# Performance work log

Measured on AMD Instinct MI355X. Metric: run time of the kernel, lower is better.

The kernel has to match this reference:

```python
import jax, jax.numpy as jnp
import numpy as np
from jax import lax

STRIDES = (8, 16, 32)
FEAT_SIZES = ((80, 80), (40, 40), (20, 20))  # 640x640 input
NUM_CLASSES = 80
NMS_THR = 0.65
SCORE_THR = 0.01
NMS_PRE = 1000
MAX_PER_IMG = 100


def make_points():
    # MlvlPointGenerator.grid_priors with offset=0, with_stride=True.
    pts = []
    for (h, w), s in zip(FEAT_SIZES, STRIDES):
        y, x = jnp.meshgrid(jnp.arange(h, dtype=jnp.float32),
                            jnp.arange(w, dtype=jnp.float32), indexing='ij')
        pts.append(jnp.stack([x.ravel() * s, y.ravel() * s,
                              jnp.full(h * w, float(s)),
                              jnp.full(h * w, float(s))], axis=-1))
    return jnp.concatenate(pts, axis=0)  # [P, 4] = (px, py, sx, sy)


def decode_boxes(points, reg):
    # YOLOXBBoxDecoder: xy = reg[:2]*stride + point; wh = exp(reg[2:])*stride
    xys = reg[..., :2] * points[..., 2:] + points[..., :2]
    whs = jnp.exp(reg[..., 2:]) * points[..., 2:]
    half = whs * 0.5
    return jnp.concatenate([xys - half, xys + half], axis=-1)  # [..., 4] xyxy


def pairwise_iou(b):
    # b: [N, 4] xyxy
    area = (b[:, 2] - b[:, 0]) * (b[:, 3] - b[:, 1])
    lt = jnp.maximum(b[:, None, :2], b[None, :, :2])
    rb = jnp.minimum(b[:, None, 2:], b[None, :, 2:])
    wh = jnp.clip(rb - lt, 0.0)
    inter = wh[..., 0] * wh[..., 1]
    return inter / (area[:, None] + area[None, :] - inter + 1e-9)


def nms_image(cls_s, boxes, obj):
    # cls_s: [P, C] sigmoid scores, boxes: [P, 4], obj: [P] sigmoid objectness
    max_scores = jnp.max(cls_s, axis=-1)
    labels = jnp.argmax(cls_s, axis=-1)
    scores = max_scores * obj
    masked = jnp.where(scores >= SCORE_THR, scores, -1.0)
    top_scores, top_idx = lax.top_k(masked, NMS_PRE)  # sorted descending
    valid = top_scores >= SCORE_THR
    b = boxes[top_idx]            # [K, 4]
    lab = labels[top_idx]         # [K]
    # batched_nms: offset boxes per class so cross-class boxes never overlap
    off = lab.astype(b.dtype)[:, None] * (jnp.max(jnp.abs(b)) + 1.0)
    iou = pairwise_iou(b + off)   # [K, K]
    idx = jnp.arange(NMS_PRE)

    def body(i, keep):
        sup = (iou[i] > NMS_THR) & keep[i] & (idx > i)
        return keep & ~sup

    keep = lax.fori_loop(0, NMS_PRE, body, valid)
    # compact kept detections (score-sorted order preserved), pad to MAX_PER_IMG
    order = jnp.argsort(~keep, stable=True)[:MAX_PER_IMG]
    k = keep[order]
    out_b = jnp.where(k[:, None], b[order], 0.0)
    out_s = jnp.where(k, top_scores[order], 0.0)
    out_l = jnp.where(k, lab[order], -1)
    return out_b, out_s, out_l


def setup_inputs() -> dict:
    key = jax.random.key(0)
    ks = jax.random.split(key, 9)
    shapes = {
        'cls0': (32, NUM_CLASSES, 80, 80), 'cls1': (32, NUM_CLASSES, 40, 40),
        'cls2': (32, NUM_CLASSES, 20, 20),
        'reg0': (32, 4, 80, 80), 'reg1': (32, 4, 40, 40), 'reg2': (32, 4, 20, 20),
        'obj0': (32, 1, 80, 80), 'obj1': (32, 1, 40, 40), 'obj2': (32, 1, 20, 20),
    }
    return {n: jax.random.normal(k, s, dtype=jnp.float32)
            for (n, s), k in zip(shapes.items(), ks)}


def reference(cls0, cls1, cls2, reg0, reg1, reg2, obj0, obj1, obj2):
    def flat(xs, c):
        return jnp.concatenate(
            [jnp.transpose(x, (0, 2, 3, 1)).reshape(x.shape[0], -1, c) for x in xs],
            axis=1)
    cls = flat([cls0, cls1, cls2], NUM_CLASSES)   # [N, P, C]
    reg = flat([reg0, reg1, reg2], 4)             # [N, P, 4]
    obj = flat([obj0, obj1, obj2], 1)[..., 0]     # [N, P]
    points = make_points()                        # [P, 4]
    boxes = decode_boxes(points[None], reg)       # [N, P, 4]
    cls = jax.nn.sigmoid(cls)
    obj = jax.nn.sigmoid(obj)
    return jax.vmap(nms_image)(cls, boxes, obj)   # ([N,M,4],[N,M],[N,M] labels)
```

## Files before the change

kernel.cpp:

```cpp
#include <hip/hip_runtime.h>
#include <stdint.h>

#define N_IMG 32
#define P_TOT 8400
#define NCLS 80
#define NMS_PRE 1000
#define MAXOUT 100
#define SCORE_THRF 0.01f
#define NMS_THRF 0.65f
#define CAND_N 2048
#define NB 512
#define BINBASE 8192
#define TIE_EPS 0.05f


__device__ __forceinline__ float sigmoidf_(float x) { return 1.0f / (1.0f + expf(-x)); }

__global__ __launch_bounds__(256) void k_score(
    const float* __restrict__ cls0, const float* __restrict__ cls1, const float* __restrict__ cls2,
    const float* __restrict__ obj0, const float* __restrict__ obj1, const float* __restrict__ obj2,
    uint64_t* __restrict__ keys)
{
    __shared__ float    pml[4][64];
    __shared__ uint64_t part[4][64];
    int lane = threadIdx.x & 63, wid = threadIdx.x >> 6;
    int a = blockIdx.x * 64 + lane;
    int n = a / P_TOT;
    int p = a - n * P_TOT;

    const float* cl; const float* ob; int HW, q;
    if (p < 6400)      { cl = cls0; ob = obj0; HW = 6400; q = p; }
    else if (p < 8000) { cl = cls1; ob = obj1; HW = 1600; q = p - 6400; }
    else               { cl = cls2; ob = obj2; HW = 400;  q = p - 8000; }

    const float* cbase = cl + (size_t)n * NCLS * HW + q;
    int c0 = wid * 20;

    float lg[20];
    #pragma unroll
    for (int i = 0; i < 20; ++i)
        lg[i] = cbase[(size_t)(c0 + i) * HW];
    __builtin_amdgcn_sched_group_barrier(0x20, 20, 0);

    float a0 = fmaxf(lg[0], lg[1]),  a1 = fmaxf(lg[2], lg[3]);
    float a2 = fmaxf(lg[4], lg[5]),  a3 = fmaxf(lg[6], lg[7]);
    float a4 = fmaxf(lg[8], lg[9]),  a5 = fmaxf(lg[10], lg[11]);
    float a6 = fmaxf(lg[12], lg[13]), a7 = fmaxf(lg[14], lg[15]);
    float a8 = fmaxf(lg[16], lg[17]), a9 = fmaxf(lg[18], lg[19]);
    float b0 = fmaxf(a0, a1), b1 = fmaxf(a2, a3), b2 = fmaxf(a4, a5);
    float b3 = fmaxf(a6, a7), b4 = fmaxf(a8, a9);
    float lmax = fmaxf(fmaxf(fmaxf(b0, b1), fmaxf(b2, b3)), b4);
    pml[wid][lane] = lmax;
    __syncthreads();

    float gmaxl = fmaxf(fmaxf(pml[0][lane], pml[1][lane]),
                        fmaxf(pml[2][lane], pml[3][lane]));
    float thr = gmaxl - TIE_EPS;
    uint64_t m = 0;
    #pragma unroll
    for (int i = 0; i < 20; ++i) {
        if (lg[i] >= thr) {
            float s = sigmoidf_(lg[i]);
            uint64_t pk = ((uint64_t)__float_as_uint(s) << 8) | (uint32_t)(79 - (c0 + i));
            m = m > pk ? m : pk;
        }
    }
    part[wid][lane] = m;
    __syncthreads();

    if (wid == 0) {
        uint64_t m0 = part[0][lane], m1 = part[1][lane];
        uint64_t m2 = part[2][lane], m3 = part[3][lane];
        uint64_t ma = m0 > m1 ? m0 : m1, mb = m2 > m3 ? m2 : m3;
        uint64_t mm = ma > mb ? ma : mb;
        float best = __uint_as_float((uint32_t)(mm >> 8));
        int bc = 79 - (int)(mm & 0xFFu);

        float so = sigmoidf_(ob[(size_t)n * HW + q]);
        float sc = __fmul_rn(best, so);
        float masked = (sc >= SCORE_THRF) ? sc : -1.0f;
        uint32_t u = __float_as_uint(masked);
        uint32_t ord = (u & 0x80000000u) ? ~u : (u | 0x80000000u);
        uint32_t dk = ~ord;
        keys[a] = ((uint64_t)dk << 32) | (uint32_t)((p << 8) | bc);
    }
}

__global__ __launch_bounds__(1024) void k_selnms(
    const uint64_t* __restrict__ keys,
    const float* __restrict__ reg0, const float* __restrict__ reg1, const float* __restrict__ reg2,
    float* __restrict__ out)
{
    __shared__ __align__(16) char big[55712];
    __shared__ int   s_misc[2];
    __shared__ float fsh[17];
    __shared__ int   kidx[MAXOUT];

    uint16_t* bin16   = (uint16_t*)big;
    uint32_t* hist    = (uint32_t*)(big + 16800);
    uint32_t* base    = (uint32_t*)(big + 18848);
    uint32_t* fill    = (uint32_t*)(big + 20896);
    uint64_t* grouped = (uint64_t*)(big + 22944);
    uint64_t* cand    = (uint64_t*)(big + 39328);
    float4* s_obx = (float4*)big;
    float*  s_oar = (float*) (big + 16000);
    float4* s_raw = (float4*)(big + 20000);
    float2* s_sl  = (float2*)(big + 36000);

    int n = blockIdx.x, tid = threadIdx.x;
    const uint64_t* kbase = keys + (size_t)n * P_TOT;

    if (tid < NB) { hist[tid] = 0; fill[tid] = 0; }
    for (int t = tid; t < CAND_N; t += 1024) cand[t] = ~0ull;
    __syncthreads();

    #pragma unroll
    for (int it = 0; it < 9; ++it) {
        int t = tid + it * 1024;
        if (t < P_TOT) {
            uint64_t k = kbase[t];
            uint32_t dk = (uint32_t)(k >> 32);
            uint16_t v = 0;
            if (!(dk & 0x80000000u)) {
                uint32_t bin = (dk >> 17) - BINBASE;
                atomicAdd(&hist[bin], 1u);
                v = (uint16_t)(bin + 1);
            }
            bin16[t] = v;
        }
    }
    __syncthreads();

    if (tid < 64) {
        uint32_t c[8]; uint32_t s = 0;
        #pragma unroll
        for (int i = 0; i < 8; ++i) { c[i] = hist[tid * 8 + i]; s += c[i]; }
        uint32_t inc = s;
        #pragma unroll
        for (int o = 1; o < 64; o <<= 1) {
            uint32_t v = __shfl_up(inc, o);
            if (tid >= o) inc += v;
        }
        uint32_t excl = inc - s;
        uint32_t b = excl;
        #pragma unroll
        for (int i = 0; i < 8; ++i) { base[tid * 8 + i] = b; b += c[i]; }
        uint32_t total = __shfl(inc, 63);
        uint32_t target = total < (uint32_t)NMS_PRE ? total : (uint32_t)NMS_PRE;
        uint32_t cum = excl; int found = 0x7fffffff;
        #pragma unroll
        for (int i = 0; i < 8; ++i) {
            cum += c[i];
            if (found == 0x7fffffff && cum >= target && target > 0) found = tid * 8 + i;
        }
        #pragma unroll
        for (int o = 32; o > 0; o >>= 1) { int f = __shfl_xor(found, o); found = f < found ? f : found; }
        if (tid == 0) { s_misc[0] = (total > 0) ? found : -1; s_misc[1] = (int)target; }
    }
    __syncthreads();
    int Bcut = s_misc[0];

    #pragma unroll
    for (int it = 0; it < 9; ++it) {
        int t = tid + it * 1024;
        if (t < P_TOT) {
            uint16_t v = bin16[t];
            if (v != 0) {
                int bin = (int)v - 1;
                if (bin <= Bcut) {
                    uint32_t pos = base[bin] + atomicAdd(&fill[bin], 1u);
                    if (pos < CAND_N) grouped[pos] = kbase[t];
                }
            }
        }
    }
    __syncthreads();

    int ccnt = 0;
    if (Bcut >= 0) {
        uint32_t cc = base[Bcut] + hist[Bcut];
        ccnt = cc < (uint32_t)CAND_N ? (int)cc : CAND_N;
    }
    for (int s = tid; s < ccnt; s += 1024) {
        uint64_t k = grouped[s];
        uint32_t dk = (uint32_t)(k >> 32);
        int bin = (int)((dk >> 17) - BINBASE);
        uint32_t b0 = base[bin];
        uint32_t e0 = b0 + hist[bin]; if (e0 > (uint32_t)CAND_N) e0 = CAND_N;
        uint32_t r = b0;
        for (uint32_t t = b0; t < e0; ++t) r += (grouped[t] < k) ? 1u : 0u;
        if (r < (uint32_t)CAND_N) cand[r] = k;
    }
    int V = s_misc[1];
    __syncthreads();

    float4 bx = make_float4(0.f, 0.f, 0.f, 0.f);
    float scm = -1.0f, labf = 0.f, m = 0.f;
    if (tid < NMS_PRE) {
        uint64_t key = cand[tid];
        uint32_t dk = (uint32_t)(key >> 32);
        if (!(dk & 0x80000000u)) {
            uint32_t low = (uint32_t)key;
            int lab = (int)(low & 0xFFu);
            int p   = (int)(low >> 8);
            uint32_t ord = ~dk;
            scm = __uint_as_float(ord ^ 0x80000000u);

            const float* rg; int HW, q, W; float s;
            if (p < 6400)      { rg = reg0; HW = 6400; q = p;        W = 80; s = 8.f; }
            else if (p < 8000) { rg = reg1; HW = 1600; q = p - 6400; W = 40; s = 16.f; }
            else               { rg = reg2; HW = 400;  q = p - 8000; W = 20; s = 32.f; }

            float px = (float)(q % W) * s;
            float py = (float)(q / W) * s;
            const float* rb = rg + (size_t)n * 4 * HW + q;
            float dx = rb[0], dy = rb[HW], dw = rb[2 * HW], dh = rb[3 * HW];
            float cx = __fadd_rn(__fmul_rn(dx, s), px);
            float cy = __fadd_rn(__fmul_rn(dy, s), py);
            float hw = __fmul_rn(__fmul_rn(expf(dw), s), 0.5f);
            float hh = __fmul_rn(__fmul_rn(expf(dh), s), 0.5f);
            bx.x = __fsub_rn(cx, hw); bx.y = __fsub_rn(cy, hh);
            bx.z = __fadd_rn(cx, hw); bx.w = __fadd_rn(cy, hh);
            labf = (float)lab;
            m = fmaxf(fmaxf(fabsf(bx.x), fabsf(bx.y)), fmaxf(fabsf(bx.z), fabsf(bx.w)));
        }
    }

    #pragma unroll
    for (int o = 32; o > 0; o >>= 1) m = fmaxf(m, __shfl_xor(m, o));
    if ((tid & 63) == 0) fsh[tid >> 6] = m;
    __syncthreads();
    if (tid == 0) {
        float g = fsh[0];
        #pragma unroll
        for (int w = 1; w < 16; ++w) g = fmaxf(g, fsh[w]);
        fsh[16] = g;
    }
    __syncthreads();
    float gmax = fsh[16];

    if (tid < NMS_PRE) {
        float off = __fmul_rn(labf, __fadd_rn(gmax, 1.0f));
        float x1 = __fadd_rn(bx.x, off), y1 = __fadd_rn(bx.y, off);
        float x2 = __fadd_rn(bx.z, off), y2 = __fadd_rn(bx.w, off);
        s_obx[tid] = make_float4(x1, y1, x2, y2);
        s_oar[tid] = __fmul_rn(__fsub_rn(x2, x1), __fsub_rn(y2, y1));
        s_raw[tid] = bx;
        s_sl[tid]  = make_float2(scm, labf);
    }
    __syncthreads();
    if (tid >= 64) return;

    int lane = tid;
    int count = 0;
    float k1x1 = 0.f, k1y1 = 0.f, k1x2 = 0.f, k1y2 = 0.f, k1a = 0.f;
    float k2x1 = 0.f, k2y1 = 0.f, k2x2 = 0.f, k2y2 = 0.f, k2a = 0.f;

    float4 nb = s_obx[0]; float na = s_oar[0];
    for (int i = 0; i < V && count < MAXOUT; ++i) {
        float4 cb = nb; float ca = na;
        int ip = (i + 1 < V) ? i + 1 : i;
        nb = s_obx[ip]; na = s_oar[ip];

        bool sup = false;
        int c1 = count < 64 ? count : 64;
        if (lane < c1) {
            float ltx = fmaxf(k1x1, cb.x), lty = fmaxf(k1y1, cb.y);
            float rbx = fminf(k1x2, cb.z), rby = fminf(k1y2, cb.w);
            float w = fmaxf(__fsub_rn(rbx, ltx), 0.f);
            float h = fmaxf(__fsub_rn(rby, lty), 0.f);
            float inter = __fmul_rn(w, h);
            float denom = __fadd_rn(__fsub_rn(__fadd_rn(k1a, ca), inter), 1e-9f);
            sup = (inter / denom > NMS_THRF);
        }
        if (count > 64 && lane < count - 64) {
            float ltx = fmaxf(k2x1, cb.x), lty = fmaxf(k2y1, cb.y);
            float rbx = fminf(k2x2, cb.z), rby = fminf(k2y2, cb.w);
            float w = fmaxf(__fsub_rn(rbx, ltx), 0.f);
            float h = fmaxf(__fsub_rn(rby, lty), 0.f);
            float inter = __fmul_rn(w, h);
            float denom = __fadd_rn(__fsub_rn(__fadd_rn(k2a, ca), inter), 1e-9f);
            sup = sup || (inter / denom > NMS_THRF);
        }
        if (__ballot(sup) == 0ull) {
            if (lane == count)      { k1x1 = cb.x; k1y1 = cb.y; k1x2 = cb.z; k1y2 = cb.w; k1a = ca; }
            if (lane + 64 == count) { k2x1 = cb.x; k2y1 = cb.y; k2x2 = cb.z; k2y2 = cb.w; k2a = ca; }
            if (lane == 0) kidx[count] = i;
            ++count;
        }
    }

    float* ob = out;
    float* os = out + N_IMG * MAXOUT * 4;
    float* ol = os + N_IMG * MAXOUT;
    for (int mi = lane; mi < MAXOUT; mi += 64) {
        int o4 = (n * MAXOUT + mi) * 4;
        if (mi < count) {
            int i = kidx[mi];
            float4 b  = s_raw[i];
            float2 sl = s_sl[i];
            ob[o4 + 0] = b.x; ob[o4 + 1] = b.y; ob[o4 + 2] = b.z; ob[o4 + 3] = b.w;
            os[n * MAXOUT + mi] = sl.x;
            ol[n * MAXOUT + mi] = sl.y;
        } else {
            ob[o4 + 0] = 0.f; ob[o4 + 1] = 0.f; ob[o4 + 2] = 0.f; ob[o4 + 3] = 0.f;
            os[n * MAXOUT + mi] = 0.f;
            ol[n * MAXOUT + mi] = -1.f;
        }
    }
}

extern "C" void kernel_launch(void* const* d_in, const int* in_sizes, int n_in,
                              void* d_out, int out_size, void* d_ws, size_t ws_size,
                              hipStream_t stream)
{
    const float* cls0 = (const float*)d_in[0];
    const float* cls1 = (const float*)d_in[1];
    const float* cls2 = (const float*)d_in[2];
    const float* reg0 = (const float*)d_in[3];
    const float* reg1 = (const float*)d_in[4];
    const float* reg2 = (const float*)d_in[5];
    const float* obj0 = (const float*)d_in[6];
    const float* obj1 = (const float*)d_in[7];
    const float* obj2 = (const float*)d_in[8];

    uint64_t* keys = (uint64_t*)d_ws;
    float* out = (float*)d_out;

    k_score<<<(N_IMG * P_TOT) / 64, 256, 0, stream>>>(
        cls0, cls1, cls2, obj0, obj1, obj2, keys);
    k_selnms<<<N_IMG, 1024, 0, stream>>>(keys, reg0, reg1, reg2, out);
}
```

Measured before the change: 68.99 us.

## Process NMS candidates in 64-wide column chunks with lane-parallel suppression

The greedy NMS loop changes from one candidate per iteration, tested against the kept boxes held in registers, to chunks of 64 candidates with one candidate per lane. Each lane first tests its candidate against all previously kept boxes, read back by index from shared memory. It then resolves suppression inside the chunk serially, using shuffles and ballots. This cuts the number of serial iterations with ballot and branch overhead for candidates that get suppressed, but every chunk repeats the test against all kept boxes from LDS, so the work grows with count times the number of chunks.

New measurement: 72.02 us. +4.4%, slower.

```diff
diff --git a/kernel.cpp b/kernel.cpp
--- a/kernel.cpp
+++ b/kernel.cpp
@@ -253,40 +253,46 @@
 
     int lane = tid;
     int count = 0;
-    float k1x1 = 0.f, k1y1 = 0.f, k1x2 = 0.f, k1y2 = 0.f, k1a = 0.f;
-    float k2x1 = 0.f, k2y1 = 0.f, k2x2 = 0.f, k2y2 = 0.f, k2a = 0.f;
-
-    float4 nb = s_obx[0]; float na = s_oar[0];
-    for (int i = 0; i < V && count < MAXOUT; ++i) {
-        float4 cb = nb; float ca = na;
-        int ip = (i + 1 < V) ? i + 1 : i;
-        nb = s_obx[ip]; na = s_oar[ip];
-
-        bool sup = false;
-        int c1 = count < 64 ? count : 64;
-        if (lane < c1) {
-            float ltx = fmaxf(k1x1, cb.x), lty = fmaxf(k1y1, cb.y);
-            float rbx = fminf(k1x2, cb.z), rby = fminf(k1y2, cb.w);
+    int nchunk = (V + 63) >> 6;
+    for (int c = 0; c < nchunk && count < MAXOUT; ++c) {
+        int jcol = (c << 6) + lane;
+        bool colv = jcol < V;
+        int jsafe = colv ? jcol : 0;
+        float4 bj = s_obx[jsafe];
+        float  aj = s_oar[jsafe];
+
+        bool sup0 = false;
+        for (int mm = 0; mm < count; ++mm) {
+            int r = kidx[mm];
+            float4 bi = s_obx[r]; float ai = s_oar[r];
+            float ltx = fmaxf(bi.x, bj.x), lty = fmaxf(bi.y, bj.y);
+            float rbx = fminf(bi.z, bj.z), rby = fminf(bi.w, bj.w);
             float w = fmaxf(__fsub_rn(rbx, ltx), 0.f);
             float h = fmaxf(__fsub_rn(rby, lty), 0.f);
             float inter = __fmul_rn(w, h);
-            float denom = __fadd_rn(__fsub_rn(__fadd_rn(k1a, ca), inter), 1e-9f);
-            sup = (inter / denom > NMS_THRF);
-        }
-        if (count > 64 && lane < count - 64) {
-            float ltx = fmaxf(k2x1, cb.x), lty = fmaxf(k2y1, cb.y);
-            float rbx = fminf(k2x2, cb.z), rby = fminf(k2y2, cb.w);
+            float denom = __fadd_rn(__fsub_rn(__fadd_rn(ai, aj), inter), 1e-9f);
+            sup0 = sup0 || (inter / denom > NMS_THRF);
+        }
+        uint64_t bm = __ballot(colv && sup0);
+
+        int lim = V - (c << 6); if (lim > 64) lim = 64;
+        for (int b = 0; b < lim; ++b) {
+            if ((bm >> b) & 1) continue;
+            int r = (c << 6) + b;
+            if (lane == 0) kidx[count] = r;
+            ++count;
+            float bix1 = __shfl(bj.x, b), biy1 = __shfl(bj.y, b);
+            float bix2 = __shfl(bj.z, b), biy2 = __shfl(bj.w, b);
+            float ai   = __shfl(aj,   b);
+            float ltx = fmaxf(bix1, bj.x), lty = fmaxf(biy1, bj.y);
+            float rbx = fminf(bix2, bj.z), rby = fminf(biy2, bj.w);
             float w = fmaxf(__fsub_rn(rbx, ltx), 0.f);
             float h = fmaxf(__fsub_rn(rby, lty), 0.f);
             float inter = __fmul_rn(w, h);
-            float denom = __fadd_rn(__fsub_rn(__fadd_rn(k2a, ca), inter), 1e-9f);
-            sup = sup || (inter / denom > NMS_THRF);
-        }
-        if (__ballot(sup) == 0ull) {
-            if (lane == count)      { k1x1 = cb.x; k1y1 = cb.y; k1x2 = cb.z; k1y2 = cb.w; k1a = ca; }
-            if (lane + 64 == count) { k2x1 = cb.x; k2y1 = cb.y; k2x2 = cb.z; k2y2 = cb.w; k2a = ca; }
-            if (lane == 0) kidx[count] = i;
-            ++count;
+            float denom = __fadd_rn(__fsub_rn(__fadd_rn(ai, aj), inter), 1e-9f);
+            bool sup = colv && (jcol > r) && (inter / denom > NMS_THRF);
+            bm |= __ballot(sup);
+            if (count >= MAXOUT) break;
         }
     }
 
```
